# Kernel tuning notes

Hardware: AMD Instinct MI355X
Metric: run time of the kernel (lower is better)

Reference implementation:

```python
import jax, jax.numpy as jnp
import numpy as np

NEG_SLOPE = 0.2  # DGL GATConv default negative_slope


def gat_layer(x, W, al, ar, b, src, dst):
    """One DGL-style GATConv layer. x:[N,F], W:[F,H*D], al/ar:[H,D], b:[H*D].
    Returns [N,H,D]."""
    N = x.shape[0]
    H, D = al.shape
    feat = (x @ W).reshape(N, H, D)               # projected features
    el = jnp.einsum('nhd,hd->nh', feat, al)       # src attention term
    er = jnp.einsum('nhd,hd->nh', feat, ar)       # dst attention term
    e = jax.nn.leaky_relu(el[src] + er[dst], NEG_SLOPE)   # [E,H]
    # segment softmax over destination nodes
    m = jax.ops.segment_max(e, dst, num_segments=N)       # [N,H]
    m = jnp.where(jnp.isfinite(m), m, 0.0)                # isolated nodes
    ex = jnp.exp(e - m[dst])                              # [E,H]
    denom = jax.ops.segment_sum(ex, dst, num_segments=N)  # [N,H]
    a = ex / denom[dst]                                   # [E,H]
    msg = a[:, :, None] * feat[src]                       # [E,H,D]
    rst = jax.ops.segment_sum(msg, dst, num_segments=N)   # [N,H,D]
    return rst + b.reshape(1, H, D)


def setup_inputs() -> dict:
    key = jax.random.key(0)
    ks = jax.random.split(key, 10)
    N, E = 100000, 1600000
    F_IN, H1, D1, F_OUT = 128, 8, 16, 64
    HID = H1 * D1  # 128
    features = jax.random.normal(ks[0], (N, F_IN), dtype=jnp.float32)
    src = jax.random.randint(ks[1], (E,), 0, N, dtype=jnp.int32)
    dst = jax.random.randint(ks[2], (E,), 0, N, dtype=jnp.int32)
    edge_type = jax.random.randint(ks[3], (E,), 0, 4, dtype=jnp.int32)
    s1 = 1.0 / np.sqrt(F_IN)
    s2 = 1.0 / np.sqrt(HID)
    w1 = jax.random.normal(ks[4], (F_IN, HID), dtype=jnp.float32) * s1
    al1 = jax.random.normal(ks[5], (H1, D1), dtype=jnp.float32) * 0.1
    ar1 = jax.random.normal(ks[6], (H1, D1), dtype=jnp.float32) * 0.1
    b1 = jnp.zeros((HID,), dtype=jnp.float32)
    w2 = jax.random.normal(ks[7], (HID, F_OUT), dtype=jnp.float32) * s2
    al2 = jax.random.normal(ks[8], (1, F_OUT), dtype=jnp.float32) * 0.1
    ar2 = jax.random.normal(ks[9], (1, F_OUT), dtype=jnp.float32) * 0.1
    b2 = jnp.zeros((F_OUT,), dtype=jnp.float32)
    return dict(features=features, src=src, dst=dst, edge_type=edge_type,
                w1=w1, al1=al1, ar1=ar1, b1=b1,
                w2=w2, al2=al2, ar2=ar2, b2=b2)


def reference(features, src, dst, edge_type, w1, al1, ar1, b1, w2, al2, ar2, b2):
    N = features.shape[0]
    # conv1: [N,H,D] -> flatten heads -> relu
    h = gat_layer(features, w1, al1, ar1, b1, src, dst).reshape(N, -1)
    h = jax.nn.relu(h)
    # conv2: single head -> squeeze -> relu
    h = gat_layer(h, w2, al2, ar2, b2, src, dst)[:, 0, :]
    h = jax.nn.relu(h)
    # dot-product edge predictor (u_dot_v) + sigmoid
    score = jnp.einsum('ed,ed->e', h[src], h[dst])
    return jax.nn.sigmoid(score)
```

## Files before the change

### kernel.cpp

```cpp
#include <hip/hip_runtime.h>
#include <math.h>

#define F_IN 128
#define HID 128
#define H1 8
#define D1 16
#define F_OUT 64

#define BSHIFT 7
#define NPB 128
#define CH 4096
#define CAP 4096

typedef unsigned int uint;
typedef unsigned short ushort;

typedef __bf16 bf16x8 __attribute__((ext_vector_type(8)));
typedef float f32x4 __attribute__((ext_vector_type(4)));
typedef float f32x2 __attribute__((ext_vector_type(2)));

__device__ __forceinline__ float bf2f(ushort u) {
  uint v = ((uint)u) << 16;
  return __builtin_bit_cast(float, v);
}
__device__ __forceinline__ ushort f2bf(float f) {
  uint u = __builtin_bit_cast(uint, f);
  u = (u + 0x7FFFu + ((u >> 16) & 1u)) >> 16;
  return (ushort)u;
}
__device__ __forceinline__ f32x2 bfpair(uint w) {
  f32x2 r;
  r.x = __builtin_bit_cast(float, w << 16);
  r.y = __builtin_bit_cast(float, w & 0xFFFF0000u);
  return r;
}


__global__ __launch_bounds__(256) void k1_scatter_gemm(
    const int* __restrict__ src, const int* __restrict__ dst,
    int* __restrict__ bcursor, uint* __restrict__ pairs, int E, int nb, int nsb,
    const float* __restrict__ X, const float* __restrict__ W,
    ushort* __restrict__ Y, int nrows) {
  __shared__ uint smem[8192];
  int t = threadIdx.x;
  if ((int)blockIdx.x < nsb) {
    int* cnt_l = (int*)smem;
    int* base_l = cnt_l + 1024;
    int* off_l = cnt_l + 2048;
    for (int i = t; i < nb; i += 256) { cnt_l[i] = 0; off_l[i] = 0; }
    __syncthreads();
    int e0 = blockIdx.x * CH;
#pragma unroll 4
    for (int k = 0; k < CH / 256; ++k) {
      int e = e0 + k * 256 + t;
      if (e < E) atomicAdd(&cnt_l[dst[e] >> BSHIFT], 1);
    }
    __syncthreads();
    for (int i = t; i < nb; i += 256)
      base_l[i] = cnt_l[i] ? atomicAdd(&bcursor[i], cnt_l[i]) : 0;
    __syncthreads();
#pragma unroll 4
    for (int k = 0; k < CH / 256; ++k) {
      int e = e0 + k * 256 + t;
      if (e < E) {
        int d = dst[e], b = d >> BSHIFT;
        int o = base_l[b] + atomicAdd(&off_l[b], 1);
        if (o < CAP) pairs[(size_t)b * CAP + o] = ((uint)(d & (NPB - 1)) << 25) | (uint)src[e];
      }
    }
  } else {
    constexpr int COLS = HID, NCT = COLS / 16;
    ushort* wlds = (ushort*)smem;
    constexpr int ITER = (128 * COLS) / 512;
#pragma unroll
    for (int it = 0; it < ITER; ++it) {
      int idx = it * 512 + t * 2;
      float2 wv = *(const float2*)(W + idx);
      int k = idx / COLS, c = idx % COLS;
      int tt = k >> 5, kb = (k >> 3) & 3, j = k & 7;
      wlds[(((tt * NCT + (c >> 4)) * 64) + ((c & 15) | (kb << 4))) * 8 + j] = f2bf(wv.x);
      int c1 = c + 1;
      wlds[(((tt * NCT + (c1 >> 4)) * 64) + ((c1 & 15) | (kb << 4))) * 8 + j] = f2bf(wv.y);
    }
    __syncthreads();
    int wid = t >> 6, lane = t & 63;
    long r0 = (long)(blockIdx.x - nsb) * 256 + wid * 64;
    if (r0 >= nrows) return;
    int lr = lane & 15, kb = lane >> 4;
    long ar4[4];
#pragma unroll
    for (int mi = 0; mi < 4; ++mi) {
      long r = r0 + mi * 16 + lr;
      ar4[mi] = (r < nrows) ? r : (long)(nrows - 1);
    }
    f32x4 acc[4][NCT];
#pragma unroll
    for (int mi = 0; mi < 4; ++mi)
#pragma unroll
      for (int ct = 0; ct < NCT; ++ct) acc[mi][ct] = (f32x4){0.f, 0.f, 0.f, 0.f};
#pragma unroll
    for (int tt = 0; tt < 4; ++tt) {
      bf16x8 af[4];
#pragma unroll
      for (int mi = 0; mi < 4; ++mi) {
        const float* xp = X + ar4[mi] * 128 + tt * 32 + kb * 8;
        float4 u = *(const float4*)xp;
        float4 v = *(const float4*)(xp + 4);
        bf16x8 a;
        a[0] = (__bf16)u.x; a[1] = (__bf16)u.y; a[2] = (__bf16)u.z; a[3] = (__bf16)u.w;
        a[4] = (__bf16)v.x; a[5] = (__bf16)v.y; a[6] = (__bf16)v.z; a[7] = (__bf16)v.w;
        af[mi] = a;
      }
#pragma unroll
      for (int ct = 0; ct < NCT; ++ct) {
        bf16x8 bf = *(const bf16x8*)&wlds[((tt * NCT + ct) * 64 + lane) * 8];
#pragma unroll
        for (int mi = 0; mi < 4; ++mi)
          acc[mi][ct] = __builtin_amdgcn_mfma_f32_16x16x32_bf16(af[mi], bf, acc[mi][ct], 0, 0, 0);
      }
    }
#pragma unroll
    for (int mi = 0; mi < 4; ++mi) {
#pragma unroll
      for (int ct = 0; ct < NCT; ++ct) {
#pragma unroll
        for (int reg = 0; reg < 4; ++reg) {
          long r = r0 + mi * 16 + kb * 4 + reg;
          if (r < nrows) Y[r * COLS + ct * 16 + lr] = f2bf(acc[mi][ct][reg]);
        }
      }
    }
  }
}


__global__ __launch_bounds__(256) void k2_build_elr(
    const uint* __restrict__ pairs, const int* __restrict__ bcursor,
    int* __restrict__ row_ptr, int* __restrict__ src_sorted, int nn, int total, int nb,
    const ushort* __restrict__ feat, const float* __restrict__ al,
    const float* __restrict__ ar, ushort* __restrict__ el, float* __restrict__ er) {
  int t = threadIdx.x;
  if ((int)blockIdx.x < nb) {
    __shared__ int h[NPB], pref[NPB], red[256];
    int b = blockIdx.x;
    int part = 0;
    for (int i = t; i < b; i += 256) part += bcursor[i];
    red[t] = part;
    __syncthreads();
    for (int off = 128; off > 0; off >>= 1) {
      if (t < off) red[t] += red[t + off];
      __syncthreads();
    }
    int csr_base = red[0];
    if (t < NPB) h[t] = 0;
    __syncthreads();
    size_t lo = (size_t)b * CAP;
    int cnt = bcursor[b];
    for (int e = t; e < cnt; e += 256) atomicAdd(&h[pairs[lo + e] >> 25], 1);
    __syncthreads();
    if (t < NPB) pref[t] = h[t];
    __syncthreads();
    for (int off = 1; off < NPB; off <<= 1) {
      int v = (t >= off && t < NPB) ? pref[t - off] : 0;
      __syncthreads();
      if (t < NPB) pref[t] += v;
      __syncthreads();
    }
    int node_base = b << BSHIFT;
    int nodes = min(NPB, nn - node_base);
    if (t < nodes) {
      int ex = csr_base + pref[t] - h[t];
      row_ptr[node_base + t] = ex;
      h[t] = ex;
    }
    __syncthreads();
    for (int e = t; e < cnt; e += 256) {
      uint p = pairs[lo + e];
      int pos = atomicAdd(&h[p >> 25], 1);
      src_sorted[pos] = (int)(p & 0x1FFFFFFu);
    }
    if (b == 0 && t == 0) row_ptr[nn] = total;
  } else {
    int idx = ((int)blockIdx.x - nb) * 256 + t;
    if (idx >= nn * H1) return;
    int n = idx >> 3, h = idx & 7;
    const uint4* f4 = (const uint4*)(feat + (size_t)n * HID + h * D1);
    const float* a = al + h * D1;
    const float* r = ar + h * D1;
    f32x2 sl2 = {0.f, 0.f}, sr2 = {0.f, 0.f};
#pragma unroll
    for (int j = 0; j < 2; ++j) {
      uint4 v = f4[j];
      uint ws[4] = {v.x, v.y, v.z, v.w};
#pragma unroll
      for (int k = 0; k < 4; ++k) {
        int d = j * 8 + k * 2;
        f32x2 f = bfpair(ws[k]);
        sl2 += f * *(const f32x2*)(a + d);
        sr2 += f * *(const f32x2*)(r + d);
      }
    }
    el[idx] = f2bf(sl2.x + sl2.y);
    er[idx] = sr2.x + sr2.y;
  }
}


template <int COLS, bool ABF16, bool FUSE_ELR>
__global__ __launch_bounds__(256) void mfma_gemm(const void* __restrict__ Xv,
                                                 const float* __restrict__ W,
                                                 ushort* __restrict__ Y,
                                                 const float* __restrict__ al,
                                                 const float* __restrict__ ar,
                                                 float* __restrict__ el,
                                                 float* __restrict__ er, int nrows) {
  constexpr int NCT = COLS / 16;
  __shared__ ushort wlds[128 * COLS];
  constexpr int ITER = (128 * COLS) / 512;
#pragma unroll
  for (int it = 0; it < ITER; ++it) {
    int idx = it * 512 + (int)threadIdx.x * 2;
    float2 wv = *(const float2*)(W + idx);
    int k = idx / COLS, c = idx % COLS;
    int t = k >> 5, kb = (k >> 3) & 3, j = k & 7;
    wlds[(((t * NCT + (c >> 4)) * 64) + ((c & 15) | (kb << 4))) * 8 + j] = f2bf(wv.x);
    int c1 = c + 1;
    wlds[(((t * NCT + (c1 >> 4)) * 64) + ((c1 & 15) | (kb << 4))) * 8 + j] = f2bf(wv.y);
  }
  __syncthreads();

  int wid = threadIdx.x >> 6, lane = threadIdx.x & 63;
  long r0 = (long)blockIdx.x * 256 + wid * 64;
  if (r0 >= nrows) return;
  int lr = lane & 15, kb = lane >> 4;
  long ar4[4];
#pragma unroll
  for (int mi = 0; mi < 4; ++mi) {
    long r = r0 + mi * 16 + lr;
    ar4[mi] = (r < nrows) ? r : (long)(nrows - 1);
  }
  f32x4 acc[4][NCT];
#pragma unroll
  for (int mi = 0; mi < 4; ++mi)
#pragma unroll
    for (int ct = 0; ct < NCT; ++ct) acc[mi][ct] = (f32x4){0.f, 0.f, 0.f, 0.f};

#pragma unroll
  for (int t = 0; t < 4; ++t) {
    bf16x8 af[4];
#pragma unroll
    for (int mi = 0; mi < 4; ++mi) {
      if constexpr (ABF16) {
        const ushort* xp = (const ushort*)Xv + ar4[mi] * 128 + t * 32 + kb * 8;
        af[mi] = *(const bf16x8*)xp;
      } else {
        const float* xp = (const float*)Xv + ar4[mi] * 128 + t * 32 + kb * 8;
        float4 u = *(const float4*)xp;
        float4 v = *(const float4*)(xp + 4);
        bf16x8 a;
        a[0] = (__bf16)u.x; a[1] = (__bf16)u.y; a[2] = (__bf16)u.z; a[3] = (__bf16)u.w;
        a[4] = (__bf16)v.x; a[5] = (__bf16)v.y; a[6] = (__bf16)v.z; a[7] = (__bf16)v.w;
        af[mi] = a;
      }
    }
#pragma unroll
    for (int ct = 0; ct < NCT; ++ct) {
      bf16x8 bf = *(const bf16x8*)&wlds[((t * NCT + ct) * 64 + lane) * 8];
#pragma unroll
      for (int mi = 0; mi < 4; ++mi)
        acc[mi][ct] = __builtin_amdgcn_mfma_f32_16x16x32_bf16(af[mi], bf, acc[mi][ct], 0, 0, 0);
    }
  }

#pragma unroll
  for (int mi = 0; mi < 4; ++mi) {
#pragma unroll
    for (int ct = 0; ct < NCT; ++ct) {
#pragma unroll
      for (int reg = 0; reg < 4; ++reg) {
        long r = r0 + mi * 16 + kb * 4 + reg;
        if (r < nrows) Y[r * COLS + ct * 16 + lr] = f2bf(acc[mi][ct][reg]);
      }
    }
  }

  if constexpr (FUSE_ELR) {
    float alv[NCT], arv[NCT];
#pragma unroll
    for (int ct = 0; ct < NCT; ++ct) {
      alv[ct] = al[ct * 16 + lr];
      arv[ct] = ar[ct * 16 + lr];
    }
#pragma unroll
    for (int mi = 0; mi < 4; ++mi) {
#pragma unroll
      for (int reg = 0; reg < 4; ++reg) {
        float pe = 0.f, pr = 0.f;
#pragma unroll
        for (int ct = 0; ct < NCT; ++ct) {
          pe += acc[mi][ct][reg] * alv[ct];
          pr += acc[mi][ct][reg] * arv[ct];
        }
#pragma unroll
        for (int off = 1; off < 16; off <<= 1) {
          pe += __shfl_xor(pe, off);
          pr += __shfl_xor(pr, off);
        }
        long r = r0 + mi * 16 + kb * 4 + reg;
        if (lr == 0 && r < nrows) { el[r] = pe; er[r] = pr; }
      }
    }
  }
}


template <int H, int D, int VEC, bool EL_BF16>
__global__ __launch_bounds__(256) void agg_kernel(
    const ushort* __restrict__ feat, const void* __restrict__ elv,
    const float* __restrict__ er, const int* __restrict__ row_ptr,
    const int* __restrict__ src_sorted, const float* __restrict__ bias,
    ushort* __restrict__ out, int nn) {
  constexpr int F = H * D;
  constexpr int LPG = 16;
  constexpr int CHUNK = 32;
  static_assert(F == LPG * VEC, "lane layout");
  int w = threadIdx.x >> 6, lane = threadIdx.x & 63;
  int g = lane >> 4, li = lane & 15;
  int n = blockIdx.x * 16 + w * 4 + g;
  __shared__ float p_sh[4][4][H][CHUNK + 2];
  __shared__ int s_sh[4][4][CHUNK + 2];
  bool node_ok = n < nn;
  int start = 0, deg = 0;
  if (node_ok) {
    start = row_ptr[n];
    deg = row_ptr[n + 1] - start;
  }
  int d0 = li * VEC;
  int h = d0 / D;
  float er_reg[H];
#pragma unroll
  for (int q = 0; q < H; ++q) er_reg[q] = 0.f;
  if (node_ok) {
    if constexpr (H == 8) {
      float4 e0 = *(const float4*)(er + (size_t)n * 8);
      float4 e1 = *(const float4*)(er + (size_t)n * 8 + 4);
      er_reg[0] = e0.x; er_reg[1] = e0.y; er_reg[2] = e0.z; er_reg[3] = e0.w;
      er_reg[4] = e1.x; er_reg[5] = e1.y; er_reg[6] = e1.z; er_reg[7] = e1.w;
    } else {
      er_reg[0] = er[n];
    }
  }
  float L = 0.f;
  f32x2 acc2[VEC / 2];
#pragma unroll
  for (int v = 0; v < VEC / 2; ++v) acc2[v] = (f32x2){0.f, 0.f};

  for (int c0 = 0; c0 < deg; c0 += CHUNK) {
    int cnt = min(CHUNK, deg - c0);
    int e0i = c0 + 2 * li;
    int2 s2 = make_int2(0, 0);
    if (e0i + 1 < deg) s2 = *(const int2*)(src_sorted + start + e0i);
    else if (e0i < deg) s2.x = src_sorted[start + e0i];
    *(int2*)&s_sh[w][g][2 * li] = s2;
#pragma unroll
    for (int half = 0; half < 2; ++half) {
      int s = half ? s2.y : s2.x;
      bool valid = (e0i + half) < deg;
      float p8[H];
      if (valid) {
        if constexpr (H == 8) {
          float ev[8];
          if constexpr (EL_BF16) {
            uint4 q4 = *(const uint4*)((const ushort*)elv + (size_t)s * 8);
            uint qs[4] = {q4.x, q4.y, q4.z, q4.w};
#pragma unroll
            for (int k = 0; k < 4; ++k) {
              f32x2 f = bfpair(qs[k]);
              ev[2 * k] = f.x;
              ev[2 * k + 1] = f.y;
            }
          } else {
            float4 e0 = *(const float4*)((const float*)elv + (size_t)s * 8);
            float4 e1 = *(const float4*)((const float*)elv + (size_t)s * 8 + 4);
            ev[0] = e0.x; ev[1] = e0.y; ev[2] = e0.z; ev[3] = e0.w;
            ev[4] = e1.x; ev[5] = e1.y; ev[6] = e1.z; ev[7] = e1.w;
          }
#pragma unroll
          for (int q = 0; q < 8; ++q) {
            float v = ev[q] + er_reg[q];
            v = v > 0.f ? v : 0.2f * v;
            p8[q] = __expf(v);
          }
        } else {
          float v = ((const float*)elv)[s] + er_reg[0];
          v = v > 0.f ? v : 0.2f * v;
          p8[0] = __expf(v);
        }
      } else {
#pragma unroll
        for (int q = 0; q < H; ++q) p8[q] = 0.f;
      }
#pragma unroll
      for (int q = 0; q < H; ++q) p_sh[w][g][q][2 * li + half] = p8[q];
    }
    __builtin_amdgcn_wave_barrier();
    const ushort* fb = feat + d0;
    int j = 0;
    for (; j + 3 < cnt; j += 4) {
      int sa = s_sh[w][g][j], sb = s_sh[w][g][j + 1];
      int sc = s_sh[w][g][j + 2], sd = s_sh[w][g][j + 3];
      float pa = p_sh[w][g][h][j], pb = p_sh[w][g][h][j + 1];
      float pc = p_sh[w][g][h][j + 2], pd = p_sh[w][g][h][j + 3];
      L += pa + pb + pc + pd;
      f32x2 Pa = {pa, pa}, Pb = {pb, pb}, Pc = {pc, pc}, Pd = {pd, pd};
      if constexpr (VEC == 8) {
        uint4 va = *(const uint4*)(fb + (size_t)sa * F);
        uint4 vb = *(const uint4*)(fb + (size_t)sb * F);
        uint4 vc = *(const uint4*)(fb + (size_t)sc * F);
        uint4 vd = *(const uint4*)(fb + (size_t)sd * F);
        acc2[0] += Pa * bfpair(va.x) + Pb * bfpair(vb.x) + Pc * bfpair(vc.x) + Pd * bfpair(vd.x);
        acc2[1] += Pa * bfpair(va.y) + Pb * bfpair(vb.y) + Pc * bfpair(vc.y) + Pd * bfpair(vd.y);
        acc2[2] += Pa * bfpair(va.z) + Pb * bfpair(vb.z) + Pc * bfpair(vc.z) + Pd * bfpair(vd.z);
        acc2[3] += Pa * bfpair(va.w) + Pb * bfpair(vb.w) + Pc * bfpair(vc.w) + Pd * bfpair(vd.w);
      } else {
        uint2 va = *(const uint2*)(fb + (size_t)sa * F);
        uint2 vb = *(const uint2*)(fb + (size_t)sb * F);
        uint2 vc = *(const uint2*)(fb + (size_t)sc * F);
        uint2 vd = *(const uint2*)(fb + (size_t)sd * F);
        acc2[0] += Pa * bfpair(va.x) + Pb * bfpair(vb.x) + Pc * bfpair(vc.x) + Pd * bfpair(vd.x);
        acc2[1] += Pa * bfpair(va.y) + Pb * bfpair(vb.y) + Pc * bfpair(vc.y) + Pd * bfpair(vd.y);
      }
    }
    for (; j < cnt; ++j) {
      float pj = p_sh[w][g][h][j];
      int sj = s_sh[w][g][j];
      L += pj;
      f32x2 Pj = {pj, pj};
      if constexpr (VEC == 8) {
        uint4 v = *(const uint4*)(fb + (size_t)sj * F);
        acc2[0] += Pj * bfpair(v.x);
        acc2[1] += Pj * bfpair(v.y);
        acc2[2] += Pj * bfpair(v.z);
        acc2[3] += Pj * bfpair(v.w);
      } else {
        uint2 v = *(const uint2*)(fb + (size_t)sj * F);
        acc2[0] += Pj * bfpair(v.x);
        acc2[1] += Pj * bfpair(v.y);
      }
    }
    __builtin_amdgcn_wave_barrier();
  }

  if (!node_ok) return;
  float inv = (L > 0.f) ? 1.f / L : 0.f;
  ushort us[VEC];
#pragma unroll
  for (int v = 0; v < VEC / 2; ++v) {
    us[2 * v] = f2bf(fmaxf(acc2[v].x * inv + bias[d0 + 2 * v], 0.f));
    us[2 * v + 1] = f2bf(fmaxf(acc2[v].y * inv + bias[d0 + 2 * v + 1], 0.f));
  }
  if constexpr (VEC == 4) {
    ushort4 u4 = {us[0], us[1], us[2], us[3]};
    *(ushort4*)&out[(size_t)n * F + d0] = u4;
  } else {
    ushort4 u40 = {us[0], us[1], us[2], us[3]};
    ushort4 u41 = {us[4], us[5], us[6], us[7]};
    *(ushort4*)&out[(size_t)n * F + d0] = u40;
    *(ushort4*)&out[(size_t)n * F + d0 + 4] = u41;
  }
}


__global__ void score_kernel(const ushort* __restrict__ h2, const int* __restrict__ src,
                             const int* __restrict__ dst, float* __restrict__ out, int E) {
  int tid = blockIdx.x * blockDim.x + threadIdx.x;
  int e = tid >> 2, sub = tid & 3;
  if (e >= E) return;
  int s = src[e], d = dst[e];
  const ushort* sp = h2 + (size_t)s * F_OUT + sub * 16;
  const ushort* dp = h2 + (size_t)d * F_OUT + sub * 16;
  uint4 a0 = *(const uint4*)sp;
  uint4 a1 = *(const uint4*)(sp + 8);
  uint4 b0 = *(const uint4*)dp;
  uint4 b1 = *(const uint4*)(dp + 8);
  uint aw[8] = {a0.x, a0.y, a0.z, a0.w, a1.x, a1.y, a1.z, a1.w};
  uint bw[8] = {b0.x, b0.y, b0.z, b0.w, b1.x, b1.y, b1.z, b1.w};
  f32x2 acc2 = {0.f, 0.f};
#pragma unroll
  for (int k = 0; k < 8; ++k) acc2 += bfpair(aw[k]) * bfpair(bw[k]);
  float p = acc2.x + acc2.y;
  p += __shfl_xor(p, 1);
  p += __shfl_xor(p, 2);
  if (sub == 0) out[e] = 1.f / (1.f + __expf(-p));
}


extern "C" void kernel_launch(void* const* d_in, const int* in_sizes, int n_in,
                              void* d_out, int out_size, void* d_ws, size_t ws_size,
                              hipStream_t stream) {
  const float* features = (const float*)d_in[0];
  const int* src = (const int*)d_in[1];
  const int* dst = (const int*)d_in[2];
  const float* w1 = (const float*)d_in[4];
  const float* al1 = (const float*)d_in[5];
  const float* ar1 = (const float*)d_in[6];
  const float* b1 = (const float*)d_in[7];
  const float* w2 = (const float*)d_in[8];
  const float* al2 = (const float*)d_in[9];
  const float* ar2 = (const float*)d_in[10];
  const float* b2 = (const float*)d_in[11];
  float* out = (float*)d_out;
  const int N = in_sizes[0] / F_IN;
  const int E = in_sizes[1];

  const int NB = (N + NPB - 1) >> BSHIFT;
  const int NSB = (E + CH - 1) / CH;
  const int gblocks = (N + 255) / 256;

  char* ws = (char*)d_ws;
  size_t off = 0;
  auto alloc = [&](size_t bytes) {
    void* p = ws + off;
    off = (off + bytes + 255) & ~(size_t)255;
    return p;
  };
  int* row_ptr = (int*)alloc((size_t)(N + 1) * 4);
  int* src_sorted = (int*)alloc((size_t)E * 4);
  int* bcursor = (int*)alloc((size_t)1024 * 4);
  uint* pairs = (uint*)alloc((size_t)NB * CAP * 4);
  ushort* feat1 = (ushort*)alloc((size_t)N * HID * 2);
  ushort* el1 = (ushort*)alloc((size_t)N * H1 * 2);
  float* er1 = (float*)alloc((size_t)N * H1 * 4);
  ushort* h1b = (ushort*)alloc((size_t)N * HID * 2);
  ushort* h2 = (ushort*)alloc((size_t)N * F_OUT * 2);
  float* el2 = (float*)alloc((size_t)N * 4);
  float* er2 = (float*)alloc((size_t)N * 4);
  ushort* feat2 = feat1;

  hipMemsetAsync(bcursor, 0, (size_t)1024 * 4, stream);
  k1_scatter_gemm<<<NSB + gblocks, 256, 0, stream>>>(
      src, dst, bcursor, pairs, E, NB, NSB, features, w1, feat1, N);
  k2_build_elr<<<NB + (N * H1 + 255) / 256, 256, 0, stream>>>(
      pairs, bcursor, row_ptr, src_sorted, N, E, NB, feat1, al1, ar1, el1, er1);
  agg_kernel<H1, D1, 8, true><<<(N + 15) / 16, 256, 0, stream>>>(
      feat1, el1, er1, row_ptr, src_sorted, b1, h1b, N);
  mfma_gemm<F_OUT, true, true><<<gblocks, 256, 0, stream>>>(
      h1b, w2, feat2, al2, ar2, el2, er2, N);
  agg_kernel<1, F_OUT, 4, false><<<(N + 15) / 16, 256, 0, stream>>>(
      feat2, el2, er2, row_ptr, src_sorted, b2, h2, N);
  {
    long threads = (long)E * 4;
    int blocks = (int)((threads + 255) / 256);
    score_kernel<<<blocks, 256, 0, stream>>>(h2, src, dst, out, E);
  }
}
```

Baseline: 227.2 us.

## Sort destination nodes by in-degree to balance aggregation work

Builds a per-degree histogram while constructing the CSR, scans it in descending-degree order, and scatters node ids into a node_order permutation. Both aggregation kernels then process nodes in this order, so each wave handles nodes of similar degree. The aim is less divergence and idle time from mixed-degree groups within a wave, at the cost of two extra small kernel launches and an indirect node lookup that breaks sequential row_ptr and output access.

```diff
diff --git a/kernel.cpp b/kernel.cpp
--- a/kernel.cpp
+++ b/kernel.cpp
@@ -11,6 +11,8 @@
 #define NPB 128
 #define CH 4096
 #define CAP 4096
+#define NBIN 32
+#define NREP 16
 
 typedef unsigned int uint;
 typedef unsigned short ushort;
@@ -136,12 +138,13 @@
 
 __global__ __launch_bounds__(256) void k2_build_elr(
     const uint* __restrict__ pairs, const int* __restrict__ bcursor,
-    int* __restrict__ row_ptr, int* __restrict__ src_sorted, int nn, int total, int nb,
+    int* __restrict__ row_ptr, int* __restrict__ src_sorted, int* __restrict__ dcnt,
+    int nn, int total, int nb,
     const ushort* __restrict__ feat, const float* __restrict__ al,
     const float* __restrict__ ar, ushort* __restrict__ el, float* __restrict__ er) {
   int t = threadIdx.x;
   if ((int)blockIdx.x < nb) {
-    __shared__ int h[NPB], pref[NPB], red[256];
+    __shared__ int h[NPB], pref[NPB], red[256], lh[NBIN];
     int b = blockIdx.x;
     int part = 0;
     for (int i = t; i < b; i += 256) part += bcursor[i];
@@ -153,21 +156,24 @@
     }
     int csr_base = red[0];
     if (t < NPB) h[t] = 0;
+    if (t < NBIN) lh[t] = 0;
     __syncthreads();
     size_t lo = (size_t)b * CAP;
     int cnt = bcursor[b];
     for (int e = t; e < cnt; e += 256) atomicAdd(&h[pairs[lo + e] >> 25], 1);
     __syncthreads();
+    int node_base = b << BSHIFT;
+    int nodes = min(NPB, nn - node_base);
+    if (t < nodes) atomicAdd(&lh[min(h[t], NBIN - 1)], 1);
     if (t < NPB) pref[t] = h[t];
     __syncthreads();
+    if (t < NBIN && lh[t]) atomicAdd(&dcnt[t * NREP + (b & (NREP - 1))], lh[t]);
     for (int off = 1; off < NPB; off <<= 1) {
       int v = (t >= off && t < NPB) ? pref[t - off] : 0;
       __syncthreads();
       if (t < NPB) pref[t] += v;
       __syncthreads();
     }
-    int node_base = b << BSHIFT;
-    int nodes = min(NPB, nn - node_base);
     if (t < nodes) {
       int ex = csr_base + pref[t] - h[t];
       row_ptr[node_base + t] = ex;
@@ -202,6 +208,47 @@
     }
     el[idx] = f2bf(sl2.x + sl2.y);
     er[idx] = sr2.x + sr2.y;
+  }
+}
+
+__global__ void order_scan(int* __restrict__ d) {
+  __shared__ int s[NBIN * NREP];
+  int t = threadIdx.x;
+  int bin = t / NREP, rep = t % NREP;
+  int key = (NBIN - 1 - bin) * NREP + rep;
+  int v = d[t];
+  s[key] = v;
+  __syncthreads();
+  for (int off = 1; off < NBIN * NREP; off <<= 1) {
+    int u = (key >= off) ? s[key - off] : 0;
+    __syncthreads();
+    s[key] += u;
+    __syncthreads();
+  }
+  d[t] = s[key] - v;
+}
+
+__global__ __launch_bounds__(128) void order_scatter(const int* __restrict__ row_ptr,
+                                                     int* __restrict__ dcur,
+                                                     int* __restrict__ node_order, int nn) {
+  __shared__ int lhist[NBIN], lbase[NBIN], lcur[NBIN];
+  int b = blockIdx.x, t = threadIdx.x;
+  if (t < NBIN) { lhist[t] = 0; lcur[t] = 0; }
+  __syncthreads();
+  int node_base = b << BSHIFT;
+  int nodes = min(NPB, nn - node_base);
+  int bin = 0;
+  if (t < nodes) {
+    int deg = row_ptr[node_base + t + 1] - row_ptr[node_base + t];
+    bin = min(deg, NBIN - 1);
+    atomicAdd(&lhist[bin], 1);
+  }
+  __syncthreads();
+  if (t < NBIN && lhist[t]) lbase[t] = atomicAdd(&dcur[t * NREP + (b & (NREP - 1))], lhist[t]);
+  __syncthreads();
+  if (t < nodes) {
+    int pos = lbase[bin] + atomicAdd(&lcur[bin], 1);
+    node_order[pos] = node_base + t;
   }
 }
 
@@ -318,20 +365,21 @@
 __global__ __launch_bounds__(256) void agg_kernel(
     const ushort* __restrict__ feat, const void* __restrict__ elv,
     const float* __restrict__ er, const int* __restrict__ row_ptr,
-    const int* __restrict__ src_sorted, const float* __restrict__ bias,
-    ushort* __restrict__ out, int nn) {
+    const int* __restrict__ src_sorted, const int* __restrict__ node_order,
+    const float* __restrict__ bias, ushort* __restrict__ out, int nn) {
   constexpr int F = H * D;
   constexpr int LPG = 16;
   constexpr int CHUNK = 32;
   static_assert(F == LPG * VEC, "lane layout");
   int w = threadIdx.x >> 6, lane = threadIdx.x & 63;
   int g = lane >> 4, li = lane & 15;
-  int n = blockIdx.x * 16 + w * 4 + g;
+  int idx = blockIdx.x * 16 + w * 4 + g;
   __shared__ float p_sh[4][4][H][CHUNK + 2];
   __shared__ int s_sh[4][4][CHUNK + 2];
-  bool node_ok = n < nn;
-  int start = 0, deg = 0;
+  bool node_ok = idx < nn;
+  int n = 0, start = 0, deg = 0;
   if (node_ok) {
+    n = node_order[idx];
     start = row_ptr[n];
     deg = row_ptr[n + 1] - start;
   }
@@ -526,7 +574,9 @@
   };
   int* row_ptr = (int*)alloc((size_t)(N + 1) * 4);
   int* src_sorted = (int*)alloc((size_t)E * 4);
-  int* bcursor = (int*)alloc((size_t)1024 * 4);
+  int* bcursor = (int*)alloc((size_t)1536 * 4);
+  int* dcnt = bcursor + 1024;
+  int* node_order = (int*)alloc((size_t)N * 4);
   uint* pairs = (uint*)alloc((size_t)NB * CAP * 4);
   ushort* feat1 = (ushort*)alloc((size_t)N * HID * 2);
   ushort* el1 = (ushort*)alloc((size_t)N * H1 * 2);
@@ -537,17 +587,19 @@
   float* er2 = (float*)alloc((size_t)N * 4);
   ushort* feat2 = feat1;
 
-  hipMemsetAsync(bcursor, 0, (size_t)1024 * 4, stream);
+  hipMemsetAsync(bcursor, 0, (size_t)1536 * 4, stream);
   k1_scatter_gemm<<<NSB + gblocks, 256, 0, stream>>>(
       src, dst, bcursor, pairs, E, NB, NSB, features, w1, feat1, N);
   k2_build_elr<<<NB + (N * H1 + 255) / 256, 256, 0, stream>>>(
-      pairs, bcursor, row_ptr, src_sorted, N, E, NB, feat1, al1, ar1, el1, er1);
+      pairs, bcursor, row_ptr, src_sorted, dcnt, N, E, NB, feat1, al1, ar1, el1, er1);
+  order_scan<<<1, NBIN * NREP, 0, stream>>>(dcnt);
+  order_scatter<<<NB, 128, 0, stream>>>(row_ptr, dcnt, node_order, N);
   agg_kernel<H1, D1, 8, true><<<(N + 15) / 16, 256, 0, stream>>>(
-      feat1, el1, er1, row_ptr, src_sorted, b1, h1b, N);
+      feat1, el1, er1, row_ptr, src_sorted, node_order, b1, h1b, N);
   mfma_gemm<F_OUT, true, true><<<gblocks, 256, 0, stream>>>(
       h1b, w2, feat2, al2, ar2, el2, er2, N);
   agg_kernel<1, F_OUT, 4, false><<<(N + 15) / 16, 256, 0, stream>>>(
-      feat2, el2, er2, row_ptr, src_sorted, b2, h2, N);
+      feat2, el2, er2, row_ptr, src_sorted, node_order, b2, h2, N);
   {
     long threads = (long)E * 4;
     int blocks = (int)((threads + 255) / 256);
```

New measurement: 257.1 us. 13.2% more time.

## Use coarse 1024-node buckets with 8-way sub-cursors for CSR build

Applied to the files above, without the earlier changes.

The destination bucketing moves from 782 buckets of 128 nodes to 98 super-buckets of 1024 nodes, each split into 8 sub-lists chosen by scatter block index to spread global cursor atomics. The CSR build then runs one block per super-bucket, scanning 1024 node counts with a 256-thread prefix scan. The aim is fewer per-block bucket counters and fewer global atomics in the scatter phase. The cost is only 98 blocks doing the CSR sort, each handling about 16K edges, so that phase has much less parallelism. Each sub-list is capped at 4096 entries, which the random test graph is not expected to exceed.

```diff
diff --git a/kernel.cpp b/kernel.cpp
--- a/kernel.cpp
+++ b/kernel.cpp
@@ -7,10 +7,10 @@
 #define D1 16
 #define F_OUT 64
 
-#define BSHIFT 7
-#define NPB 128
+#define SBSHIFT 10
+#define SNPB 1024
 #define CH 4096
-#define CAP 4096
+#define SCAP8 4096
 
 typedef unsigned int uint;
 typedef unsigned short ushort;
@@ -36,36 +36,40 @@
 }
 
 
+
 __global__ __launch_bounds__(256) void k1_scatter_gemm(
     const int* __restrict__ src, const int* __restrict__ dst,
-    int* __restrict__ bcursor, uint* __restrict__ pairs, int E, int nb, int nsb,
+    int* __restrict__ bcursor, uint* __restrict__ pairs, int E, int snb, int nsb,
     const float* __restrict__ X, const float* __restrict__ W,
     ushort* __restrict__ Y, int nrows) {
   __shared__ uint smem[8192];
   int t = threadIdx.x;
   if ((int)blockIdx.x < nsb) {
     int* cnt_l = (int*)smem;
-    int* base_l = cnt_l + 1024;
-    int* off_l = cnt_l + 2048;
-    for (int i = t; i < nb; i += 256) { cnt_l[i] = 0; off_l[i] = 0; }
+    int* base_l = cnt_l + 128;
+    int* off_l = cnt_l + 256;
+    int xg = blockIdx.x & 7;
+    for (int i = t; i < snb; i += 256) { cnt_l[i] = 0; off_l[i] = 0; }
     __syncthreads();
     int e0 = blockIdx.x * CH;
 #pragma unroll 4
     for (int k = 0; k < CH / 256; ++k) {
       int e = e0 + k * 256 + t;
-      if (e < E) atomicAdd(&cnt_l[dst[e] >> BSHIFT], 1);
-    }
-    __syncthreads();
-    for (int i = t; i < nb; i += 256)
-      base_l[i] = cnt_l[i] ? atomicAdd(&bcursor[i], cnt_l[i]) : 0;
+      if (e < E) atomicAdd(&cnt_l[dst[e] >> SBSHIFT], 1);
+    }
+    __syncthreads();
+    for (int i = t; i < snb; i += 256)
+      base_l[i] = cnt_l[i] ? atomicAdd(&bcursor[i * 8 + xg], cnt_l[i]) : 0;
     __syncthreads();
 #pragma unroll 4
     for (int k = 0; k < CH / 256; ++k) {
       int e = e0 + k * 256 + t;
       if (e < E) {
-        int d = dst[e], b = d >> BSHIFT;
+        int d = dst[e], b = d >> SBSHIFT;
         int o = base_l[b] + atomicAdd(&off_l[b], 1);
-        if (o < CAP) pairs[(size_t)b * CAP + o] = ((uint)(d & (NPB - 1)) << 25) | (uint)src[e];
+        if (o < SCAP8)
+          pairs[((size_t)b * 8 + xg) * SCAP8 + o] =
+              ((uint)(d & (SNPB - 1)) << 22) | (uint)src[e];
       }
     }
   } else {
@@ -136,15 +140,18 @@
 
 __global__ __launch_bounds__(256) void k2_build_elr(
     const uint* __restrict__ pairs, const int* __restrict__ bcursor,
-    int* __restrict__ row_ptr, int* __restrict__ src_sorted, int nn, int total, int nb,
+    int* __restrict__ row_ptr, int* __restrict__ src_sorted,
+    int nn, int total, int snb,
     const ushort* __restrict__ feat, const float* __restrict__ al,
     const float* __restrict__ ar, ushort* __restrict__ el, float* __restrict__ er) {
   int t = threadIdx.x;
-  if ((int)blockIdx.x < nb) {
-    __shared__ int h[NPB], pref[NPB], red[256];
+  if ((int)blockIdx.x < snb) {
+    __shared__ int h[SNPB];
+    __shared__ int red[256];
     int b = blockIdx.x;
+    int lim = b * 8;
     int part = 0;
-    for (int i = t; i < b; i += 256) part += bcursor[i];
+    for (int i = t; i < lim; i += 256) part += bcursor[i];
     red[t] = part;
     __syncthreads();
     for (int off = 128; off > 0; off >>= 1) {
@@ -152,41 +159,55 @@
       __syncthreads();
     }
     int csr_base = red[0];
-    if (t < NPB) h[t] = 0;
-    __syncthreads();
-    size_t lo = (size_t)b * CAP;
-    int cnt = bcursor[b];
-    for (int e = t; e < cnt; e += 256) atomicAdd(&h[pairs[lo + e] >> 25], 1);
-    __syncthreads();
-    if (t < NPB) pref[t] = h[t];
-    __syncthreads();
-    for (int off = 1; off < NPB; off <<= 1) {
-      int v = (t >= off && t < NPB) ? pref[t - off] : 0;
+    __syncthreads();
+#pragma unroll
+    for (int k = 0; k < 4; ++k) h[t + k * 256] = 0;
+    __syncthreads();
+    for (int xg = 0; xg < 8; ++xg) {
+      int cnt = bcursor[lim + xg];
+      const uint* pp = pairs + ((size_t)lim + xg) * SCAP8;
+      for (int e = t; e < cnt; e += 256) atomicAdd(&h[pp[e] >> 22], 1);
+    }
+    __syncthreads();
+    int c0 = h[4 * t], c1 = h[4 * t + 1], c2 = h[4 * t + 2], c3 = h[4 * t + 3];
+    int s = c0 + c1 + c2 + c3;
+    red[t] = s;
+    __syncthreads();
+    for (int off = 1; off < 256; off <<= 1) {
+      int u = (t >= off) ? red[t - off] : 0;
       __syncthreads();
-      if (t < NPB) pref[t] += v;
+      red[t] += u;
       __syncthreads();
     }
-    int node_base = b << BSHIFT;
-    int nodes = min(NPB, nn - node_base);
-    if (t < nodes) {
-      int ex = csr_base + pref[t] - h[t];
-      row_ptr[node_base + t] = ex;
-      h[t] = ex;
-    }
-    __syncthreads();
-    for (int e = t; e < cnt; e += 256) {
-      uint p = pairs[lo + e];
-      int pos = atomicAdd(&h[p >> 25], 1);
-      src_sorted[pos] = (int)(p & 0x1FFFFFFu);
+    int ex = red[t] - s;
+    int node_base = b << SBSHIFT;
+    int g0 = csr_base + ex;
+    int g1 = g0 + c0, g2 = g1 + c1, g3 = g2 + c2;
+    h[4 * t] = g0; h[4 * t + 1] = g1; h[4 * t + 2] = g2; h[4 * t + 3] = g3;
+#pragma unroll
+    for (int k = 0; k < 4; ++k) {
+      int idx = 4 * t + k;
+      int gv = (k == 0) ? g0 : (k == 1) ? g1 : (k == 2) ? g2 : g3;
+      if (node_base + idx < nn) row_ptr[node_base + idx] = gv;
+    }
+    __syncthreads();
+    for (int xg = 0; xg < 8; ++xg) {
+      int cnt = bcursor[lim + xg];
+      const uint* pp = pairs + ((size_t)lim + xg) * SCAP8;
+      for (int e = t; e < cnt; e += 256) {
+        uint p = pp[e];
+        int pos = atomicAdd(&h[p >> 22], 1);
+        src_sorted[pos] = (int)(p & 0x3FFFFFu);
+      }
     }
     if (b == 0 && t == 0) row_ptr[nn] = total;
   } else {
-    int idx = ((int)blockIdx.x - nb) * 256 + t;
+    int idx = ((int)blockIdx.x - snb) * 256 + t;
     if (idx >= nn * H1) return;
-    int n = idx >> 3, h = idx & 7;
-    const uint4* f4 = (const uint4*)(feat + (size_t)n * HID + h * D1);
-    const float* a = al + h * D1;
-    const float* r = ar + h * D1;
+    int n = idx >> 3, h2i = idx & 7;
+    const uint4* f4 = (const uint4*)(feat + (size_t)n * HID + h2i * D1);
+    const float* a = al + h2i * D1;
+    const float* r = ar + h2i * D1;
     f32x2 sl2 = {0.f, 0.f}, sr2 = {0.f, 0.f};
 #pragma unroll
     for (int j = 0; j < 2; ++j) {
@@ -513,7 +534,7 @@
   const int N = in_sizes[0] / F_IN;
   const int E = in_sizes[1];
 
-  const int NB = (N + NPB - 1) >> BSHIFT;
+  const int SNB = (N + SNPB - 1) >> SBSHIFT;
   const int NSB = (E + CH - 1) / CH;
   const int gblocks = (N + 255) / 256;
 
@@ -527,7 +548,7 @@
   int* row_ptr = (int*)alloc((size_t)(N + 1) * 4);
   int* src_sorted = (int*)alloc((size_t)E * 4);
   int* bcursor = (int*)alloc((size_t)1024 * 4);
-  uint* pairs = (uint*)alloc((size_t)NB * CAP * 4);
+  uint* pairs = (uint*)alloc((size_t)SNB * 8 * SCAP8 * 4);
   ushort* feat1 = (ushort*)alloc((size_t)N * HID * 2);
   ushort* el1 = (ushort*)alloc((size_t)N * H1 * 2);
   float* er1 = (float*)alloc((size_t)N * H1 * 4);
@@ -539,9 +560,9 @@
 
   hipMemsetAsync(bcursor, 0, (size_t)1024 * 4, stream);
   k1_scatter_gemm<<<NSB + gblocks, 256, 0, stream>>>(
-      src, dst, bcursor, pairs, E, NB, NSB, features, w1, feat1, N);
-  k2_build_elr<<<NB + (N * H1 + 255) / 256, 256, 0, stream>>>(
-      pairs, bcursor, row_ptr, src_sorted, N, E, NB, feat1, al1, ar1, el1, er1);
+      src, dst, bcursor, pairs, E, SNB, NSB, features, w1, feat1, N);
+  k2_build_elr<<<SNB + (N * H1 + 255) / 256, 256, 0, stream>>>(
+      pairs, bcursor, row_ptr, src_sorted, N, E, SNB, feat1, al1, ar1, el1, er1);
   agg_kernel<H1, D1, 8, true><<<(N + 15) / 16, 256, 0, stream>>>(
       feat1, el1, er1, row_ptr, src_sorted, b1, h1b, N);
   mfma_gemm<F_OUT, true, true><<<gblocks, 256, 0, stream>>>(
```

Result: slower. 255.4 us (+12.4%).
